# Optimization experiments

Measured on AMD Instinct MI355X. Metric: run time of the kernel, lower is better.

Reference implementation:

```python
import jax, jax.numpy as jnp
import numpy as np

B, M, GRID = 4, 8192, 32          # batches, points per batch, voxel grid side
N = B * M
K = 8                              # knn neighbors (includes self at dist 0)
C_IN, C_OUT, H = 8, 8, 128
KEYB = 64                          # hash base (coords shifted +1 stay in [0,33])
EPS = 1e-5


def setup_inputs() -> dict:
    rng = np.random.default_rng(0)
    # unique occupied voxels per batch (ME SparseTensor requires unique coords)
    cs = []
    for b in range(B):
        lin = rng.choice(GRID ** 3, size=M, replace=False)
        x, y, z = lin // (GRID * GRID), (lin // GRID) % GRID, lin % GRID
        cs.append(np.stack([np.full(M, b), x, y, z], axis=1))
    coords = jnp.asarray(np.concatenate(cs, axis=0).astype(np.int32))  # [N,4]

    key = jax.random.key(0)
    ks = jax.random.split(key, 4)
    feats = jax.random.normal(ks[0], (N, C_IN), jnp.float32)
    w1 = jax.random.normal(ks[1], ((K + 1) * C_IN, H), jnp.float32) * 0.05  # 1x1 conv
    g1 = jnp.ones((H,), jnp.float32)
    b1 = jnp.zeros((H,), jnp.float32)
    w3 = jax.random.normal(ks[2], (27, H, H), jnp.float32) * 0.02          # 3^3 sparse conv
    g2 = jnp.ones((H,), jnp.float32)
    b2 = jnp.zeros((H,), jnp.float32)
    w_out = jax.random.normal(ks[3], (H, 2 * C_OUT), jnp.float32) * 0.05   # 1x1 conv
    return dict(coords=coords, feats=feats, w1=w1, g1=g1, b1=b1,
                w3=w3, g2=g2, b2=b2, w_out=w_out)


def _knn_idx(coords):
    # per-batch brute-force kNN on xyz (batch column segments the search)
    xyz = coords[:, 1:].astype(jnp.float32).reshape(B, M, 3)
    d2 = jnp.sum((xyz[:, :, None, :] - xyz[:, None, :, :]) ** 2, -1)  # [B,M,M]
    _, idx = jax.lax.top_k(-d2, K)                                     # [B,M,K]
    return (idx + (jnp.arange(B) * M)[:, None, None]).reshape(N, K)


def _bn(x, g, b):
    mu = jnp.mean(x, axis=0)
    var = jnp.var(x, axis=0)
    return (x - mu) * jax.lax.rsqrt(var + EPS) * g + b


def reference(coords, feats, w1, g1, b1, w3, g2, b2, w_out):
    # --- kNN gather-and-build: [center || k neighbor feats] -> (k+1)*C_in ---
    nbr = _knn_idx(coords)                                        # [N,K] int
    combined = jnp.concatenate([feats[:, None, :], feats[nbr]], axis=1)
    combined = combined.reshape(N, (K + 1) * C_IN)
    # --- neighbor_processor: 1x1 conv + BN + ReLU ---
    h = jax.nn.relu(_bn(combined @ w1, g1, b1))                   # [N,H]
    # --- context_predictor conv k=3: gather inputs at coord+offset via hash ---
    c = coords[:, 1:] + 1                                         # shift so offsets stay >= 0
    keys = ((coords[:, 0] * KEYB + c[:, 0]) * KEYB + c[:, 1]) * KEYB + c[:, 2]
    order = jnp.argsort(keys)
    skeys = keys[order]
    offs = jnp.stack(jnp.meshgrid(*([jnp.arange(-1, 2)] * 3), indexing='ij'),
                     axis=-1).reshape(27, 3)                      # {-1,0,1}^3
    okey = (offs[:, 0] * KEYB + offs[:, 1]) * KEYB + offs[:, 2]   # [27]
    q = keys[None, :] + okey[:, None]                             # [27,N]
    pos = jnp.clip(jnp.searchsorted(skeys, q), 0, N - 1)
    valid = skeys[pos] == q                                       # [27,N]
    j = order[pos]                                                # [27,N]
    gathered = jnp.where(valid[..., None], h[j], 0.0)             # [27,N,H]
    h2 = jnp.einsum('onc,ocd->nd', gathered, w3)                  # [N,H]
    h2 = jax.nn.relu(_bn(h2, g2, b2))
    # --- final 1x1 conv -> mean/scale ---
    return h2 @ w_out                                             # [N, 2*C_OUT]
```

## Files before the change

kernel.cpp:

```cpp
#include <hip/hip_runtime.h>
#include <hip/hip_bf16.h>

#define B_   4
#define M_   8192
#define N_   32768
#define H_   128
#define EPS_ 1e-5f
#define TBL  1048576
#define GUARD 8192

typedef short short8 __attribute__((ext_vector_type(8)));
typedef float f32x4  __attribute__((ext_vector_type(4)));

__global__ __launch_bounds__(256) void prep_kernel(const int* __restrict__ coords,
                                                   int* __restrict__ table,
                                                   int* __restrict__ packed,
                                                   int* __restrict__ keyb,
                                                   float* __restrict__ gsum,
                                                   unsigned int* __restrict__ hbz) {
    int n = blockIdx.x * 256 + threadIdx.x;
    int b = coords[4*n+0], x = coords[4*n+1], y = coords[4*n+2], z = coords[4*n+3];
    packed[n] = (x << 10) | (y << 5) | z;
    int key = ((b*64 + x+1)*64 + y+1)*64 + (z+1);
    keyb[n] = key;
    table[key] = n;
    if (blockIdx.x == 0) gsum[threadIdx.x] = 0.f;
    if (blockIdx.x == 1 && threadIdx.x < 64) hbz[threadIdx.x] = 0u;
}

__global__ __launch_bounds__(256) void w3pack_kernel(const float* __restrict__ w3,
                                                     ushort* __restrict__ w3f) {
    int t = blockIdx.x * 256 + threadIdx.x;
    int lane = t & 63;
    int ct   = (t >> 6) & 7;
    int ks   = (t >> 9) & 3;
    int o    = t >> 11;
    int quad = lane >> 4, l15 = lane & 15;
    int n = ct*16 + l15;
    const float* src = w3 + o*16384;
    ushort out8[8];
#pragma unroll
    for (int j = 0; j < 8; ++j) {
        int c = ks*32 + quad*8 + j;
        float v = src[c*128 + n];
        __hip_bfloat16 bv = __float2bfloat16(v);
        ushort u; __builtin_memcpy(&u, &bv, 2);
        out8[j] = u;
    }
    *(uint4*)&w3f[t*8] = *(uint4*)out8;
}

__global__ __launch_bounds__(256) void knn_window_kernel(const int* __restrict__ table,
                                                         const int* __restrict__ keyb,
                                                         int* __restrict__ nbr,
                                                         int* __restrict__ flagcnt,
                                                         int* __restrict__ flaglist) {
    __shared__ int okey_sh[125], d2_sh[125];
    __shared__ int tops[256 * 8];
    int tid = threadIdx.x;
    if (tid < 125) {
        int dx = tid / 25 - 2, rr = tid % 25, dy = rr / 5 - 2, dz = rr % 5 - 2;
        okey_sh[tid] = dx * 4096 + dy * 64 + dz;
        d2_sh[tid]   = dx*dx + dy*dy + dz*dz;
    }
    __syncthreads();

    int q   = blockIdx.x * 64 + (tid >> 2);
    int sub = tid & 3;
    int kb  = keyb[q];

    int top[8];
#pragma unroll
    for (int k = 0; k < 8; ++k) top[k] = 0x7FFFFFFF;

    int base = sub * 32;
    int cnt  = (sub == 3) ? 29 : 32;
    for (int i = 0; i < cnt; ++i) {
        int idx = base + i;
        int j = table[kb + okey_sh[idx]];
        if (j >= 0) {
            int key = (d2_sh[idx] << 13) | (j & 8191);
            if (key < top[7]) {
#pragma unroll
                for (int k = 7; k >= 1; --k)
                    top[k] = (key < top[k]) ? max(key, top[k-1]) : top[k];
                top[0] = min(key, top[0]);
            }
        }
    }
#pragma unroll
    for (int k = 0; k < 8; ++k) tops[tid*8 + k] = top[k];
    __syncthreads();

    if (sub == 0) {
        const int* L = &tops[tid*8];
        int ia0 = 0, ia1 = 0, ia2 = 0, ia3 = 0;
        int res[8];
#pragma unroll
        for (int k = 0; k < 8; ++k) {
            int v0 = L[ia0], v1 = L[8 + ia1], v2 = L[16 + ia2], v3 = L[24 + ia3];
            int m01 = min(v0, v1), m23 = min(v2, v3);
            int m = min(m01, m23);
            res[k] = m;
            if (m == v0) ++ia0; else if (m == v1) ++ia1;
            else if (m == v2) ++ia2; else ++ia3;
        }
        int bb = q & ~(M_-1);
        if ((res[7] >> 13) <= 8) {
#pragma unroll
            for (int k = 0; k < 8; ++k) nbr[q*8 + k] = bb + (res[k] & 8191);
        } else {
            int pos = atomicAdd(flagcnt, 1);
            flaglist[pos] = q;
        }
    }
}

__global__ __launch_bounds__(256) void knn_bf_kernel(const int* __restrict__ packed,
                                                     const int* __restrict__ flagcnt,
                                                     const int* __restrict__ flaglist,
                                                     int* __restrict__ nbr) {
    __shared__ int tops[256 * 8];
    int tid = threadIdx.x;
    int cnt = *flagcnt;
    for (int f = blockIdx.x; f < cnt; f += gridDim.x) {
        int n = flaglist[f];
        int bb = n & ~(M_-1);
        int p = packed[n];
        int qx = (p >> 10) & 31, qy = (p >> 5) & 31, qz = p & 31;
        int top[8];
#pragma unroll
        for (int k = 0; k < 8; ++k) top[k] = 0x7FFFFFFF;
        for (int j = tid; j < M_; j += 256) {
            int c = packed[bb + j];
            int dx = qx - ((c >> 10) & 31);
            int dy = qy - ((c >> 5) & 31);
            int dz = qz - (c & 31);
            int d2 = dx*dx + dy*dy + dz*dz;
            int key = (d2 << 13) | j;
            if (key < top[7]) {
#pragma unroll
                for (int k = 7; k >= 1; --k)
                    top[k] = (key < top[k]) ? max(key, top[k-1]) : top[k];
                top[0] = min(key, top[0]);
            }
        }
#pragma unroll
        for (int k = 0; k < 8; ++k) tops[tid*8 + k] = top[k];
        __syncthreads();
        for (int stride = 128; stride >= 1; stride >>= 1) {
            if (tid < stride) {
                int* A  = &tops[tid*8];
                int* Bp = &tops[(tid+stride)*8];
                int r[8]; int ia = 0, ib = 0;
#pragma unroll
                for (int k = 0; k < 8; ++k) {
                    int a = A[ia], b2 = Bp[ib];
                    if (a <= b2) { r[k] = a; ++ia; } else { r[k] = b2; ++ib; }
                }
#pragma unroll
                for (int k = 0; k < 8; ++k) A[k] = r[k];
            }
            __syncthreads();
        }
        if (tid == 0) {
#pragma unroll
            for (int k = 0; k < 8; ++k) nbr[n*8 + k] = bb + (tops[k] & 8191);
        }
        __syncthreads();
    }
}

__global__ __launch_bounds__(256) void h1_kernel(const float* __restrict__ feats,
                                                 const int* __restrict__ nbr,
                                                 const float* __restrict__ w1,
                                                 float* __restrict__ hpre) {
    __shared__ float comb[16][72];
    int tid = threadIdx.x;
    int rowbase = blockIdx.x * 16;
    if (tid < 144) {
        int r = tid / 9, s = tid % 9;
        int grow = rowbase + r;
        int idx = (s == 0) ? grow : nbr[grow*8 + (s-1)];
        const float4* f = (const float4*)(feats + idx * 8);
        float4 a = f[0], b = f[1];
        float* dp = &comb[r][s*8];
        dp[0]=a.x; dp[1]=a.y; dp[2]=a.z; dp[3]=a.w;
        dp[4]=b.x; dp[5]=b.y; dp[6]=b.z; dp[7]=b.w;
    }
    __syncthreads();
    int c = tid & 127, rh = tid >> 7;
    float acc[8];
#pragma unroll
    for (int i = 0; i < 8; ++i) acc[i] = 0.f;
    for (int s = 0; s < 72; ++s) {
        float w = w1[s*128 + c];
#pragma unroll
        for (int i = 0; i < 8; ++i)
            acc[i] += comb[rh*8 + i][s] * w;
    }
#pragma unroll
    for (int i = 0; i < 8; ++i)
        hpre[(rowbase + rh*8 + i)*128 + c] = acc[i];
}

__global__ __launch_bounds__(256) void reduce_kernel(const float* __restrict__ src,
                                                     float* __restrict__ part) {
    __shared__ float ssum[256], ssq[256];
    int tid = threadIdx.x;
    int c = tid & 127, halfr = tid >> 7;
    int rowbase = blockIdx.x * 128 + halfr * 64;
    float s = 0.f, q = 0.f;
    for (int i = 0; i < 64; ++i) {
        float v = src[(rowbase + i)*128 + c];
        s += v; q += v*v;
    }
    ssum[tid] = s; ssq[tid] = q;
    __syncthreads();
    if (tid < 128) {
        part[blockIdx.x*256 + tid]       = ssum[tid] + ssum[tid+128];
        part[blockIdx.x*256 + 128 + tid] = ssq[tid]  + ssq[tid+128];
    }
}

__global__ __launch_bounds__(128) void stats_kernel(const float* __restrict__ part,
                                                    const float* __restrict__ g,
                                                    const float* __restrict__ bias,
                                                    float* __restrict__ scale,
                                                    float* __restrict__ shift) {
    int c = threadIdx.x;
    float s = 0.f, q = 0.f;
    for (int b = 0; b < 256; ++b) {
        s += part[b*256 + c];
        q += part[b*256 + 128 + c];
    }
    float mu  = s / (float)N_;
    float var = q / (float)N_ - mu*mu;
    float inv = rsqrtf(var + EPS_);
    float sc  = inv * g[c];
    scale[c] = sc;
    shift[c] = bias[c] - mu * sc;
}

__global__ __launch_bounds__(128) void stats2_kernel(const float* __restrict__ gsum,
                                                     const float* __restrict__ g,
                                                     const float* __restrict__ bias,
                                                     float* __restrict__ scale,
                                                     float* __restrict__ shift) {
    int c = threadIdx.x;
    float s = gsum[c], q = gsum[128 + c];
    float mu  = s / (float)N_;
    float var = q / (float)N_ - mu*mu;
    float inv = rsqrtf(var + EPS_);
    float sc  = inv * g[c];
    scale[c] = sc;
    shift[c] = bias[c] - mu * sc;
}

__global__ __launch_bounds__(256) void bnrelu_bf16_kernel(const float* __restrict__ x,
                                                          const float* __restrict__ scale,
                                                          const float* __restrict__ shift,
                                                          ushort* __restrict__ y) {
    int i = blockIdx.x * 256 + threadIdx.x;
    float4 v = ((const float4*)x)[i];
    int c = (i * 4) & 127;
    v.x = fmaxf(0.f, v.x*scale[c]   + shift[c]);
    v.y = fmaxf(0.f, v.y*scale[c+1] + shift[c+1]);
    v.z = fmaxf(0.f, v.z*scale[c+2] + shift[c+2]);
    v.w = fmaxf(0.f, v.w*scale[c+3] + shift[c+3]);
    ushort o[4];
#pragma unroll
    for (int k = 0; k < 4; ++k) {
        float f = (&v.x)[k];
        __hip_bfloat16 bv = __float2bfloat16(f);
        __builtin_memcpy(&o[k], &bv, 2);
    }
    ((ushort4*)y)[i] = make_ushort4(o[0], o[1], o[2], o[3]);
}

__global__ __launch_bounds__(256) void conv3_mfma_kernel(const ushort* __restrict__ hb,
                                                         const ushort* __restrict__ w3f,
                                                         const int* __restrict__ table,
                                                         const int* __restrict__ keyb,
                                                         float* __restrict__ h2,
                                                         float* __restrict__ gsum) {
    __shared__ ushort As[2][64 * 128];
    __shared__ int jsh[27 * 64];
    __shared__ int kbsh[64];
    int tid = threadIdx.x;
    int lane = tid & 63, wid = tid >> 6;
    int quad = lane >> 4, l15 = lane & 15;
    int bid = blockIdx.x;
    int swz = (bid & 7) * 64 + (bid >> 3);
    int rowbase = swz * 64;
    int rb = (wid >> 1) * 2;
    int cb = (wid & 1) * 4;

    if (tid < 64) kbsh[tid] = keyb[rowbase + tid];
    __syncthreads();
    for (int t = tid; t < 27*64; t += 256) {
        int o = t >> 6, r = t & 63;
        int dx = o/9 - 1, dy = (o/3)%3 - 1, dz = o%3 - 1;
        jsh[t] = table[kbsh[r] + dx*4096 + dy*64 + dz];
    }
    __syncthreads();

#pragma unroll
    for (int i = 0; i < 4; ++i) {
        int flat = i*256 + tid;
        int r = flat >> 4, cp = flat & 15;
        int j = jsh[r];
        const ushort* src = hb + j*128 + ((cp ^ (r & 15)) << 3);
        __builtin_amdgcn_global_load_lds(
            (const __attribute__((address_space(1))) unsigned int*)src,
            (__attribute__((address_space(3))) unsigned int*)&As[0][flat << 3],
            16, 0, 0);
    }
    __syncthreads();

    f32x4 acc[2][4];
#pragma unroll
    for (int i = 0; i < 2; ++i)
#pragma unroll
        for (int c = 0; c < 4; ++c)
            acc[i][c] = (f32x4){0.f, 0.f, 0.f, 0.f};

    int cur = 0;
#pragma unroll 1
    for (int o = 0; o < 27; ++o) {
        short8 bfr[4][4];
        const ushort* wb = w3f + (o << 14) + (cb << 9) + (lane << 3);
#pragma unroll
        for (int ks = 0; ks < 4; ++ks)
#pragma unroll
            for (int c = 0; c < 4; ++c)
                bfr[ks][c] = *(const short8*)(wb + (ks << 12) + (c << 9));
        if (o < 26) {
#pragma unroll
            for (int i = 0; i < 4; ++i) {
                int flat = i*256 + tid;
                int r = flat >> 4, cp = flat & 15;
                int j = jsh[(o+1)*64 + r];
                const ushort* src = hb + j*128 + ((cp ^ (r & 15)) << 3);
                __builtin_amdgcn_global_load_lds(
                    (const __attribute__((address_space(1))) unsigned int*)src,
                    (__attribute__((address_space(3))) unsigned int*)&As[cur ^ 1][flat << 3],
                    16, 0, 0);
            }
        }
#pragma unroll
        for (int ks = 0; ks < 4; ++ks) {
            short8 af[2];
#pragma unroll
            for (int i = 0; i < 2; ++i) {
                int lr = (rb + i)*16 + l15;
                int chunk = (ks*4 + quad) ^ l15;
                af[i] = *(const short8*)&As[cur][lr*128 + chunk*8];
            }
#pragma unroll
            for (int i = 0; i < 2; ++i)
#pragma unroll
                for (int c = 0; c < 4; ++c)
                    acc[i][c] = __builtin_amdgcn_mfma_f32_16x16x32_bf16(af[i], bfr[ks][c], acc[i][c], 0, 0, 0);
        }
        __syncthreads();
        cur ^= 1;
    }

    float s[4], q[4];
#pragma unroll
    for (int c = 0; c < 4; ++c) { s[c] = 0.f; q[c] = 0.f; }
#pragma unroll
    for (int i = 0; i < 2; ++i)
#pragma unroll
        for (int c = 0; c < 4; ++c)
#pragma unroll
            for (int r = 0; r < 4; ++r) {
                int row = rowbase + (rb + i)*16 + quad*4 + r;
                int col = (cb + c)*16 + l15;
                float v = acc[i][c][r];
                h2[row*128 + col] = v;
                s[c] += v; q[c] += v*v;
            }
    float* red = (float*)&As[0][0];
    red[tid] = 0.f;
    __syncthreads();
#pragma unroll
    for (int c = 0; c < 4; ++c) {
        int col = (cb + c)*16 + l15;
        atomicAdd(&red[col], s[c]);
        atomicAdd(&red[128 + col], q[c]);
    }
    __syncthreads();
    atomicAdd(&gsum[tid], red[tid]);
}

__global__ __launch_bounds__(256) void out_kernel(const float* __restrict__ h2,
                                                  const float* __restrict__ wout,
                                                  const float* __restrict__ scale,
                                                  const float* __restrict__ shift,
                                                  float* __restrict__ out) {
    __shared__ float sc[128], sh[128];
    int tid = threadIdx.x;
    if (tid < 128) { sc[tid] = scale[tid]; sh[tid] = shift[tid]; }
    __syncthreads();
    int r = tid >> 4, d = tid & 15;
    int row = blockIdx.x * 16 + r;
    float acc = 0.f;
    for (int c = 0; c < 128; ++c) {
        float hv = fmaxf(0.f, fmaf(h2[row*128 + c], sc[c], sh[c]));
        acc = fmaf(hv, wout[c*16 + d], acc);
    }
    out[row*16 + d] = acc;
}

extern "C" void kernel_launch(void* const* d_in, const int* in_sizes, int n_in,
                              void* d_out, int out_size, void* d_ws, size_t ws_size,
                              hipStream_t stream) {
    const int*   coords = (const int*)d_in[0];
    const float* feats  = (const float*)d_in[1];
    const float* w1     = (const float*)d_in[2];
    const float* g1     = (const float*)d_in[3];
    const float* b1     = (const float*)d_in[4];
    const float* w3     = (const float*)d_in[5];
    const float* g2     = (const float*)d_in[6];
    const float* b2     = (const float*)d_in[7];
    const float* wout   = (const float*)d_in[8];
    float* out = (float*)d_out;

    char* ws = (char*)d_ws;
    int*    table_base = (int*)(ws);
    int*    table   = table_base + GUARD;
    int*    packed  = (int*)(ws + (4352u<<10));
    int*    keyb    = (int*)(ws + (4608u<<10));
    int*    nbr     = (int*)(ws + (4864u<<10));
    int*    flagcnt = (int*)(ws + (5888u<<10));
    int*    flaglist= (int*)(ws + (5892u<<10));
    float*  part    = (float*)(ws + (6144u<<10));
    float*  scale1  = (float*)(ws + (6400u<<10));
    float*  shift1  = scale1 + 128;
    float*  scale2  = shift1 + 128;
    float*  shift2  = scale2 + 128;
    float*  gsum    = (float*)(ws + (6416u<<10));
    ushort* w3f     = (ushort*)(ws + (6656u<<10));
    ushort* hb      = (ushort*)(ws + (7680u<<10));
    float*  h       = (float*)(ws + (15872u<<10));
    float*  h2      = h;

    hipMemsetAsync(table_base, 0xFF, (TBL + GUARD) * sizeof(int), stream);
    hipMemsetAsync(flagcnt, 0, sizeof(int), stream);
    prep_kernel      <<<N_/256, 256, 0, stream>>>(coords, table, packed, keyb,
                                                  gsum, (unsigned int*)(hb - 128));
    w3pack_kernel    <<<216, 256, 0, stream>>>(w3, w3f);
    knn_window_kernel<<<N_/64, 256, 0, stream>>>(table, keyb, nbr, flagcnt, flaglist);
    knn_bf_kernel    <<<256, 256, 0, stream>>>(packed, flagcnt, flaglist, nbr);
    h1_kernel        <<<N_/16, 256, 0, stream>>>(feats, nbr, w1, h);
    reduce_kernel    <<<N_/128, 256, 0, stream>>>(h, part);
    stats_kernel     <<<1, 128, 0, stream>>>(part, g1, b1, scale1, shift1);
    bnrelu_bf16_kernel<<<(N_*H_/4)/256, 256, 0, stream>>>(h, scale1, shift1, hb);
    conv3_mfma_kernel<<<N_/64, 256, 0, stream>>>(hb, w3f, table, keyb, h2, gsum);
    stats2_kernel    <<<1, 128, 0, stream>>>(gsum, g2, b2, scale2, shift2);
    out_kernel       <<<N_/16, 256, 0, stream>>>(h2, wout, scale2, shift2, out);
}
```

Measured before the change: 239.6 us.

## Double the conv3 row tile and stage weights through LDS with async loads

The sparse 3x3x3 conv kernel now handles 128 rows per block with 512 threads instead of 64 rows with 256. Each offset's 128x128 bf16 weight slice is double-buffered in LDS with global_load_lds alongside the gathered activations, replacing per-wave register loads of weights straight from global memory. This halves the number of weight fetches per row and overlaps them with the MFMA compute. In exchange it needs about 142 KB of dynamic LDS, which allows only one block per CU and cuts the grid to 256 blocks.

```diff
diff --git a/kernel.cpp b/kernel.cpp
--- a/kernel.cpp
+++ b/kernel.cpp
@@ -278,28 +278,32 @@
     ((ushort4*)y)[i] = make_ushort4(o[0], o[1], o[2], o[3]);
 }
 
-__global__ __launch_bounds__(256) void conv3_mfma_kernel(const ushort* __restrict__ hb,
+#define CONV3_LDS 145408
+__global__ __launch_bounds__(512) void conv3_mfma_kernel(const ushort* __restrict__ hb,
                                                          const ushort* __restrict__ w3f,
                                                          const int* __restrict__ table,
                                                          const int* __restrict__ keyb,
                                                          float* __restrict__ h2,
                                                          float* __restrict__ gsum) {
-    __shared__ ushort As[2][64 * 128];
-    __shared__ int jsh[27 * 64];
-    __shared__ int kbsh[64];
+    extern __shared__ char smem_raw[];
+    ushort* Asb = (ushort*)smem_raw;
+    ushort* Bsb = (ushort*)(smem_raw + 65536);
+    int*    jsh = (int*)(smem_raw + 131072);
+    int*    kbsh= (int*)(smem_raw + 144896);
+
     int tid = threadIdx.x;
     int lane = tid & 63, wid = tid >> 6;
     int quad = lane >> 4, l15 = lane & 15;
     int bid = blockIdx.x;
-    int swz = (bid & 7) * 64 + (bid >> 3);
-    int rowbase = swz * 64;
-    int rb = (wid >> 1) * 2;
+    int swz = (bid & 7) * 32 + (bid >> 3);
+    int rowbase = swz * 128;
+    int wr = wid >> 1;
     int cb = (wid & 1) * 4;
 
-    if (tid < 64) kbsh[tid] = keyb[rowbase + tid];
-    __syncthreads();
-    for (int t = tid; t < 27*64; t += 256) {
-        int o = t >> 6, r = t & 63;
+    if (tid < 128) kbsh[tid] = keyb[rowbase + tid];
+    __syncthreads();
+    for (int t = tid; t < 27*128; t += 512) {
+        int o = t >> 7, r = t & 127;
         int dx = o/9 - 1, dy = (o/3)%3 - 1, dz = o%3 - 1;
         jsh[t] = table[kbsh[r] + dx*4096 + dy*64 + dz];
     }
@@ -307,13 +311,17 @@
 
 #pragma unroll
     for (int i = 0; i < 4; ++i) {
-        int flat = i*256 + tid;
+        int flat = i*512 + tid;
         int r = flat >> 4, cp = flat & 15;
         int j = jsh[r];
-        const ushort* src = hb + j*128 + ((cp ^ (r & 15)) << 3);
+        const ushort* asrc = hb + j*128 + ((cp ^ (r & 15)) << 3);
         __builtin_amdgcn_global_load_lds(
-            (const __attribute__((address_space(1))) unsigned int*)src,
-            (__attribute__((address_space(3))) unsigned int*)&As[0][flat << 3],
+            (const __attribute__((address_space(1))) unsigned int*)asrc,
+            (__attribute__((address_space(3))) unsigned int*)&Asb[flat << 3],
+            16, 0, 0);
+        __builtin_amdgcn_global_load_lds(
+            (const __attribute__((address_space(1))) unsigned int*)(w3f + (flat << 3)),
+            (__attribute__((address_space(3))) unsigned int*)&Bsb[flat << 3],
             16, 0, 0);
     }
     __syncthreads();
@@ -328,40 +336,45 @@
     int cur = 0;
 #pragma unroll 1
     for (int o = 0; o < 27; ++o) {
-        short8 bfr[4][4];
-        const ushort* wb = w3f + (o << 14) + (cb << 9) + (lane << 3);
-#pragma unroll
-        for (int ks = 0; ks < 4; ++ks)
+        if (o < 26) {
+            int obase = (o + 1) << 7;
+            const ushort* wsrc = w3f + ((o + 1) << 14);
+            int dst = (cur ^ 1) * 16384;
+#pragma unroll
+            for (int i = 0; i < 4; ++i) {
+                int flat = i*512 + tid;
+                int r = flat >> 4, cp = flat & 15;
+                int j = jsh[obase + r];
+                const ushort* asrc = hb + j*128 + ((cp ^ (r & 15)) << 3);
+                __builtin_amdgcn_global_load_lds(
+                    (const __attribute__((address_space(1))) unsigned int*)asrc,
+                    (__attribute__((address_space(3))) unsigned int*)&Asb[dst + (flat << 3)],
+                    16, 0, 0);
+                __builtin_amdgcn_global_load_lds(
+                    (const __attribute__((address_space(1))) unsigned int*)(wsrc + (flat << 3)),
+                    (__attribute__((address_space(3))) unsigned int*)&Bsb[dst + (flat << 3)],
+                    16, 0, 0);
+            }
+        }
+        const ushort* Ac = Asb + cur*16384;
+        const ushort* Bc = Bsb + cur*16384;
+#pragma unroll
+        for (int ks = 0; ks < 4; ++ks) {
+            short8 af[2], bfr[4];
+#pragma unroll
+            for (int i = 0; i < 2; ++i) {
+                int lr = wr*32 + i*16 + l15;
+                int chunk = (ks*4 + quad) ^ l15;
+                af[i] = *(const short8*)&Ac[lr*128 + chunk*8];
+            }
 #pragma unroll
             for (int c = 0; c < 4; ++c)
-                bfr[ks][c] = *(const short8*)(wb + (ks << 12) + (c << 9));
-        if (o < 26) {
-#pragma unroll
-            for (int i = 0; i < 4; ++i) {
-                int flat = i*256 + tid;
-                int r = flat >> 4, cp = flat & 15;
-                int j = jsh[(o+1)*64 + r];
-                const ushort* src = hb + j*128 + ((cp ^ (r & 15)) << 3);
-                __builtin_amdgcn_global_load_lds(
-                    (const __attribute__((address_space(1))) unsigned int*)src,
-                    (__attribute__((address_space(3))) unsigned int*)&As[cur ^ 1][flat << 3],
-                    16, 0, 0);
-            }
-        }
-#pragma unroll
-        for (int ks = 0; ks < 4; ++ks) {
-            short8 af[2];
-#pragma unroll
-            for (int i = 0; i < 2; ++i) {
-                int lr = (rb + i)*16 + l15;
-                int chunk = (ks*4 + quad) ^ l15;
-                af[i] = *(const short8*)&As[cur][lr*128 + chunk*8];
-            }
+                bfr[c] = *(const short8*)&Bc[((ks*8 + cb + c)*64 + lane) << 3];
 #pragma unroll
             for (int i = 0; i < 2; ++i)
 #pragma unroll
                 for (int c = 0; c < 4; ++c)
-                    acc[i][c] = __builtin_amdgcn_mfma_f32_16x16x32_bf16(af[i], bfr[ks][c], acc[i][c], 0, 0, 0);
+                    acc[i][c] = __builtin_amdgcn_mfma_f32_16x16x32_bf16(af[i], bfr[c], acc[i][c], 0, 0, 0);
         }
         __syncthreads();
         cur ^= 1;
@@ -376,14 +389,14 @@
         for (int c = 0; c < 4; ++c)
 #pragma unroll
             for (int r = 0; r < 4; ++r) {
-                int row = rowbase + (rb + i)*16 + quad*4 + r;
+                int row = rowbase + wr*32 + i*16 + quad*4 + r;
                 int col = (cb + c)*16 + l15;
                 float v = acc[i][c][r];
                 h2[row*128 + col] = v;
                 s[c] += v; q[c] += v*v;
             }
-    float* red = (float*)&As[0][0];
-    red[tid] = 0.f;
+    float* red = (float*)smem_raw;
+    if (tid < 256) red[tid] = 0.f;
     __syncthreads();
 #pragma unroll
     for (int c = 0; c < 4; ++c) {
@@ -392,7 +405,7 @@
         atomicAdd(&red[128 + col], q[c]);
     }
     __syncthreads();
-    atomicAdd(&gsum[tid], red[tid]);
+    if (tid < 256) atomicAdd(&gsum[tid], red[tid]);
 }
 
 __global__ __launch_bounds__(256) void out_kernel(const float* __restrict__ h2,
@@ -447,6 +460,13 @@
     float*  h       = (float*)(ws + (15872u<<10));
     float*  h2      = h;
 
+    static bool conv3_attr_set = false;
+    if (!conv3_attr_set) {
+        hipFuncSetAttribute(reinterpret_cast<const void*>(&conv3_mfma_kernel),
+                            hipFuncAttributeMaxDynamicSharedMemorySize, CONV3_LDS);
+        conv3_attr_set = true;
+    }
+
     hipMemsetAsync(table_base, 0xFF, (TBL + GUARD) * sizeof(int), stream);
     hipMemsetAsync(flagcnt, 0, sizeof(int), stream);
     prep_kernel      <<<N_/256, 256, 0, stream>>>(coords, table, packed, keyb,
@@ -458,7 +478,7 @@
     reduce_kernel    <<<N_/128, 256, 0, stream>>>(h, part);
     stats_kernel     <<<1, 128, 0, stream>>>(part, g1, b1, scale1, shift1);
     bnrelu_bf16_kernel<<<(N_*H_/4)/256, 256, 0, stream>>>(h, scale1, shift1, hb);
-    conv3_mfma_kernel<<<N_/64, 256, 0, stream>>>(hb, w3f, table, keyb, h2, gsum);
+    conv3_mfma_kernel<<<N_/128, 512, CONV3_LDS, stream>>>(hb, w3f, table, keyb, h2, gsum);
     stats2_kernel    <<<1, 128, 0, stream>>>(gsum, g2, b2, scale2, shift2);
     out_kernel       <<<N_/16, 256, 0, stream>>>(h2, wout, scale2, shift2, out);
 }
```

Measured after the change: 228.4 us. 1.05x faster.
